# Kernel optimization log

Hardware: AMD Instinct MI355X
Metric: run time of the kernel (lower is better)

The kernel has to match this reference:

```python
import jax, jax.numpy as jnp
import numpy as np

N = 50000
E = 800000
F_IN = 1433
H = 256
C = 7


def setup_inputs() -> dict:
    key = jax.random.key(0)
    ks = jax.random.split(key, 8)
    x = jax.random.normal(ks[0], (N, F_IN), dtype=jnp.float32)
    edge_index = jax.random.randint(ks[1], (2, E), 0, N, dtype=jnp.int32)
    # glorot init for linear weights
    def glorot(k, fan_in, fan_out):
        s = jnp.sqrt(6.0 / (fan_in + fan_out)).astype(jnp.float32)
        return jax.random.uniform(k, (fan_in, fan_out), jnp.float32, -s, s)
    W1 = glorot(ks[2], F_IN, H)
    W2 = glorot(ks[3], H, H)
    W3 = glorot(ks[4], H, C)
    b1 = jnp.zeros((H,), jnp.float32)
    b2 = jnp.zeros((H,), jnp.float32)
    b3 = jnp.zeros((C,), jnp.float32)
    return {"x": x, "edge_index": edge_index, "W1": W1, "b1": b1,
            "W2": W2, "b2": b2, "W3": W3, "b3": b3}


def _gcn_norm(edge_index, num_nodes):
    # add self-loops, edge_weight = 1, symmetric normalization
    row = jnp.concatenate([edge_index[0], jnp.arange(num_nodes, dtype=edge_index.dtype)])
    col = jnp.concatenate([edge_index[1], jnp.arange(num_nodes, dtype=edge_index.dtype)])
    w = jnp.ones(row.shape[0], dtype=jnp.float32)
    deg = jax.ops.segment_sum(w, col, num_segments=num_nodes)  # degree on target (col)
    dinv = jnp.where(deg > 0, jax.lax.rsqrt(deg), 0.0)
    norm = dinv[row] * dinv[col]  # [E+N]
    return row, col, norm


def _gcn_layer(x, W, b, row, col, norm, num_nodes):
    h = x @ W                                   # [N, F_out]
    msg = h[row] * norm[:, None]                # gather + scale, [E+N, F_out]
    out = jax.ops.segment_sum(msg, col, num_segments=num_nodes)  # scatter-add
    return out + b


def reference(x, edge_index, W1, b1, W2, b2, W3, b3):
    row, col, norm = _gcn_norm(edge_index, N)
    h = jax.nn.relu(_gcn_layer(x, W1, b1, row, col, norm, N))
    h = jax.nn.relu(_gcn_layer(h, W2, b2, row, col, norm, N))
    h = _gcn_layer(h, W3, b3, row, col, norm, N)
    return jax.nn.log_softmax(h, axis=1)
```

## Files before the change

### kernel.cpp

```cpp
#include <hip/hip_runtime.h>
#include <math.h>

#define NNODES 50000
#define NEDGES 800000
#define FIN    1433
#define KP1    1472
#define HDIM   256
#define NCLS   7
#define MPAD   50048

typedef __attribute__((ext_vector_type(8))) short short8;
typedef __attribute__((ext_vector_type(4))) float f32x4;

__device__ __forceinline__ unsigned short f2bf(float f) {
    unsigned u = __builtin_bit_cast(unsigned, f);
    u += 0x7fffu + ((u >> 16) & 1u);
    return (unsigned short)(u >> 16);
}

__device__ __forceinline__ float bf2f(unsigned short u) {
    unsigned v = ((unsigned)u) << 16;
    return __builtin_bit_cast(float, v);
}

__device__ __forceinline__ void gl2lds16(const void* g, void* l) {
    __builtin_amdgcn_global_load_lds(
        (const __attribute__((address_space(1))) unsigned int*)g,
        (__attribute__((address_space(3))) unsigned int*)l, 16, 0, 0);
}


__global__ void count_kernel(const int* __restrict__ col, int* __restrict__ cnt, int E) {
    int e = blockIdx.x * blockDim.x + threadIdx.x;
    if (e < E) atomicAdd(&cnt[col[e]], 1);
}

__global__ __launch_bounds__(1024) void scan_kernel(const int* __restrict__ cnt,
                                                    int* __restrict__ rp,
                                                    float* __restrict__ dinv,
                                                    int n, int total) {
    __shared__ int sums[1024];
    int t = threadIdx.x;
    int chunk = (n + 1023) >> 10;
    int start = t * chunk;
    int end = start + chunk; if (end > n) end = n;
    int local = 0;
    for (int j = start; j < end; ++j) local += cnt[j];
    sums[t] = local;
    __syncthreads();
    for (int off = 1; off < 1024; off <<= 1) {
        int v = (t >= off) ? sums[t - off] : 0;
        __syncthreads();
        sums[t] += v;
        __syncthreads();
    }
    int run = (t == 0) ? 0 : sums[t - 1];
    for (int j = start; j < end; ++j) {
        int c = cnt[j];
        rp[j] = run; run += c;
        dinv[j] = rsqrtf((float)(c + 1));
    }
    if (t == 0) rp[n] = total;
}

__global__ void fill_kernel(const int* __restrict__ row, const int* __restrict__ col,
                            const int* __restrict__ rp, int* __restrict__ cur,
                            int* __restrict__ csr, float* __restrict__ wcsr,
                            const float* __restrict__ dinv, int E) {
    int e = blockIdx.x * blockDim.x + threadIdx.x;
    if (e < E) {
        int c = col[e], r = row[e];
        int pos = rp[c] + atomicAdd(&cur[c], 1);
        csr[pos] = r;
        wcsr[pos] = dinv[r] * dinv[c];
    }
}


__global__ void cast_wt_kernel(const float* __restrict__ W, unsigned short* __restrict__ Wt,
                               int Kin, int Kp, int Nn) {
    int idx = blockIdx.x * blockDim.x + threadIdx.x;
    if (idx >= Nn * Kp) return;
    int n = idx / Kp, k = idx % Kp;
    float f = (k < Kin) ? W[(size_t)k * Nn + n] : 0.f;
    Wt[idx] = f2bf(f);
}


__global__ __launch_bounds__(256) void gemm1_fused(const float* __restrict__ X,
                                                   const unsigned short* __restrict__ Bt,
                                                   unsigned short* __restrict__ C) {
    __shared__ __align__(16) unsigned short As[64 * 64];
    __shared__ __align__(16) unsigned short Bs[256 * 64];
    const int tid = threadIdx.x;
    const int wave = tid >> 6, lane = tid & 63;
    const int m0 = blockIdx.x * 64;
    const int wn = wave * 64;
    const int kq = lane >> 4, l16 = lane & 15, l8 = lane & 7, lh = lane >> 3;

    int rowbase[16];
    #pragma unroll
    for (int i = 0; i < 16; ++i) {
        int r = m0 + i * 4 + wave;
        if (r >= NNODES) r = NNODES - 1;
        rowbase[i] = r * FIN;
    }
    const int aw0 = wave * 64 + ((lh ^ wave) * 8) + l8;
    const int aw1 = wave * 64 + ((lh ^ (wave + 4)) * 8) + l8;

    int bo[8];
    #pragma unroll
    for (int i = 0; i < 8; ++i) {
        int c = i * 256 + tid;
        int n = c >> 3, ccg = (c & 7) ^ (n & 7);
        bo[i] = n * KP1 + ccg * 8;
    }

    int aoffb[2], boffb[2];
    #pragma unroll
    for (int ks = 0; ks < 2; ++ks) {
        int swz = ((ks * 4 + kq) ^ (l16 & 7)) * 8;
        aoffb[ks] = l16 * 64 + swz;
        boffb[ks] = (wn + l16) * 64 + swz;
    }

    f32x4 acc[4][4] = {};
    constexpr int NT = KP1 / 64;

    float fv[16];
    {
        #pragma unroll
        for (int i = 0; i < 16; ++i) fv[i] = X[rowbase[i] + lane];
    }

    for (int t = 0; t < NT; ++t) {
        const int k0 = t * 64;
        #pragma unroll
        for (int i = 0; i < 8; ++i)
            gl2lds16(Bt + bo[i] + k0, &Bs[(i * 256 + tid) * 8]);
        #pragma unroll
        for (int i = 0; i < 16; ++i)
            As[i * 256 + ((i & 1) ? aw1 : aw0)] = f2bf(fv[i]);
        __syncthreads();

        float nv[16];
        const bool more = (t + 1 < NT);
        if (more) {
            const int k = k0 + 64 + lane;
            const bool tail = (t + 2 == NT);
            #pragma unroll
            for (int i = 0; i < 16; ++i)
                nv[i] = (!tail || k < FIN) ? X[rowbase[i] + k] : 0.f;
        }

        #pragma unroll
        for (int ks = 0; ks < 2; ++ks) {
            short8 af[4], bg[4];
            #pragma unroll
            for (int i = 0; i < 4; ++i) af[i] = *(const short8*)&As[i * 1024 + aoffb[ks]];
            #pragma unroll
            for (int j = 0; j < 4; ++j) bg[j] = *(const short8*)&Bs[j * 1024 + boffb[ks]];
            #pragma unroll
            for (int i = 0; i < 4; ++i)
                #pragma unroll
                for (int j = 0; j < 4; ++j)
                    acc[i][j] = __builtin_amdgcn_mfma_f32_16x16x32_bf16(af[i], bg[j], acc[i][j], 0, 0, 0);
        }
        __syncthreads();
        if (more) {
            #pragma unroll
            for (int i = 0; i < 16; ++i) fv[i] = nv[i];
        }
    }

    #pragma unroll
    for (int i = 0; i < 4; ++i) {
        int gm_base = m0 + i * 16 + (lane >> 4) * 4;
        #pragma unroll
        for (int r = 0; r < 4; ++r) {
            int gm = gm_base + r;
            if (gm < NNODES) {
                #pragma unroll
                for (int j = 0; j < 4; ++j) {
                    int gn = wn + j * 16 + l16;
                    C[(size_t)gm * HDIM + gn] = f2bf(acc[i][j][r]);
                }
            }
        }
    }
}


__global__ __launch_bounds__(256) void gemm2_lds(const unsigned short* __restrict__ A,
                                                 const unsigned short* __restrict__ Bt,
                                                 unsigned short* __restrict__ C) {
    __shared__ __align__(16) unsigned short As[64 * 64];
    __shared__ __align__(16) unsigned short Bs[256 * 64];
    const int tid = threadIdx.x;
    const int wave = tid >> 6, lane = tid & 63;
    const int m0 = blockIdx.x * 64;
    const int wn = wave * 64;
    const int kq = lane >> 4, l16 = lane & 15;

    int ao[2];
    #pragma unroll
    for (int i = 0; i < 2; ++i) {
        int c = i * 256 + tid;
        int m = c >> 3, ccg = (c & 7) ^ (m & 7);
        ao[i] = (m0 + m) * HDIM + ccg * 8;
    }
    int bo[8];
    #pragma unroll
    for (int i = 0; i < 8; ++i) {
        int c = i * 256 + tid;
        int n = c >> 3, ccg = (c & 7) ^ (n & 7);
        bo[i] = n * HDIM + ccg * 8;
    }
    int aoffb[2], boffb[2];
    #pragma unroll
    for (int ks = 0; ks < 2; ++ks) {
        int swz = ((ks * 4 + kq) ^ (l16 & 7)) * 8;
        aoffb[ks] = l16 * 64 + swz;
        boffb[ks] = (wn + l16) * 64 + swz;
    }

    f32x4 acc[4][4] = {};
    #pragma unroll
    for (int k0 = 0; k0 < HDIM; k0 += 64) {
        #pragma unroll
        for (int i = 0; i < 2; ++i) gl2lds16(A + ao[i] + k0, &As[(i * 256 + tid) * 8]);
        #pragma unroll
        for (int i = 0; i < 8; ++i) gl2lds16(Bt + bo[i] + k0, &Bs[(i * 256 + tid) * 8]);
        __syncthreads();
        #pragma unroll
        for (int ks = 0; ks < 2; ++ks) {
            short8 af[4], bg[4];
            #pragma unroll
            for (int i = 0; i < 4; ++i) af[i] = *(const short8*)&As[i * 1024 + aoffb[ks]];
            #pragma unroll
            for (int j = 0; j < 4; ++j) bg[j] = *(const short8*)&Bs[j * 1024 + boffb[ks]];
            #pragma unroll
            for (int i = 0; i < 4; ++i)
                #pragma unroll
                for (int j = 0; j < 4; ++j)
                    acc[i][j] = __builtin_amdgcn_mfma_f32_16x16x32_bf16(af[i], bg[j], acc[i][j], 0, 0, 0);
        }
        __syncthreads();
    }

    #pragma unroll
    for (int i = 0; i < 4; ++i) {
        int gm_base = m0 + i * 16 + (lane >> 4) * 4;
        #pragma unroll
        for (int r = 0; r < 4; ++r) {
            int gm = gm_base + r;
            if (gm < NNODES) {
                #pragma unroll
                for (int j = 0; j < 4; ++j) {
                    int gn = wn + j * 16 + l16;
                    C[(size_t)gm * HDIM + gn] = f2bf(acc[i][j][r]);
                }
            }
        }
    }
}


__device__ __forceinline__ void aggregate_row(const ushort4* __restrict__ h, int lane,
                                              int p, int p1,
                                              const int* __restrict__ csr,
                                              const float* __restrict__ wcsr,
                                              float& ax, float& ay, float& az, float& aw) {
    for (; p + 8 <= p1; p += 8) {
        int s[8]; float wv[8];
        #pragma unroll
        for (int j = 0; j < 8; ++j) { s[j] = csr[p + j]; wv[j] = wcsr[p + j]; }
        ushort4 t[8];
        #pragma unroll
        for (int j = 0; j < 8; ++j) t[j] = h[s[j] * 64 + lane];
        #pragma unroll
        for (int j = 0; j < 8; ++j) {
            ax += wv[j] * bf2f(t[j].x); ay += wv[j] * bf2f(t[j].y);
            az += wv[j] * bf2f(t[j].z); aw += wv[j] * bf2f(t[j].w);
        }
    }
    if (p + 4 <= p1) {
        int s[4]; float wv[4];
        #pragma unroll
        for (int j = 0; j < 4; ++j) { s[j] = csr[p + j]; wv[j] = wcsr[p + j]; }
        ushort4 t[4];
        #pragma unroll
        for (int j = 0; j < 4; ++j) t[j] = h[s[j] * 64 + lane];
        #pragma unroll
        for (int j = 0; j < 4; ++j) {
            ax += wv[j] * bf2f(t[j].x); ay += wv[j] * bf2f(t[j].y);
            az += wv[j] * bf2f(t[j].z); aw += wv[j] * bf2f(t[j].w);
        }
        p += 4;
    }
    for (; p < p1; ++p) {
        int s = csr[p];
        float wg = wcsr[p];
        ushort4 t = h[s * 64 + lane];
        ax += wg * bf2f(t.x); ay += wg * bf2f(t.y); az += wg * bf2f(t.z); aw += wg * bf2f(t.w);
    }
}


__global__ __launch_bounds__(256) void agg_kernel(const ushort4* __restrict__ h,
                                                  ushort4* __restrict__ out,
                                                  const float* __restrict__ dinv,
                                                  const int* __restrict__ rp,
                                                  const int* __restrict__ csr,
                                                  const float* __restrict__ wcsr,
                                                  const float* __restrict__ bias,
                                                  int n) {
    int node = blockIdx.x * 4 + (threadIdx.x >> 6);
    int lane = threadIdx.x & 63;
    if (node >= n) return;
    float di = dinv[node];
    float sw = di * di;
    ushort4 hv = h[node * 64 + lane];
    float ax = sw * bf2f(hv.x), ay = sw * bf2f(hv.y);
    float az = sw * bf2f(hv.z), aw = sw * bf2f(hv.w);
    aggregate_row(h, lane, rp[node], rp[node + 1], csr, wcsr, ax, ay, az, aw);
    float4 b = ((const float4*)bias)[lane];
    ax = fmaxf(ax + b.x, 0.f); ay = fmaxf(ay + b.y, 0.f);
    az = fmaxf(az + b.z, 0.f); aw = fmaxf(aw + b.w, 0.f);
    out[node * 64 + lane] = make_ushort4(f2bf(ax), f2bf(ay), f2bf(az), f2bf(aw));
}


__global__ __launch_bounds__(256) void agg2_mm3_kernel(const ushort4* __restrict__ h,
                                                       float* __restrict__ h3,
                                                       const float* __restrict__ dinv,
                                                       const int* __restrict__ rp,
                                                       const int* __restrict__ csr,
                                                       const float* __restrict__ wcsr,
                                                       const float* __restrict__ bias,
                                                       const float* __restrict__ W3,
                                                       int n) {
    __shared__ __align__(16) float Ws[NCLS * HDIM];
    int tid = threadIdx.x;
    for (int i = tid; i < NCLS * HDIM; i += 256)
        Ws[i] = W3[(i & 255) * NCLS + (i >> 8)];
    __syncthreads();

    int node = blockIdx.x * 4 + (tid >> 6);
    int lane = tid & 63;
    if (node >= n) return;
    float di = dinv[node];
    float sw = di * di;
    ushort4 hv = h[node * 64 + lane];
    float ax = sw * bf2f(hv.x), ay = sw * bf2f(hv.y);
    float az = sw * bf2f(hv.z), aw = sw * bf2f(hv.w);
    aggregate_row(h, lane, rp[node], rp[node + 1], csr, wcsr, ax, ay, az, aw);
    float4 b = ((const float4*)bias)[lane];
    ax = fmaxf(ax + b.x, 0.f); ay = fmaxf(ay + b.y, 0.f);
    az = fmaxf(az + b.z, 0.f); aw = fmaxf(aw + b.w, 0.f);

    float p7[NCLS];
    #pragma unroll
    for (int c = 0; c < NCLS; ++c) {
        float4 w4 = *(const float4*)&Ws[c * HDIM + 4 * lane];
        p7[c] = ax * w4.x + ay * w4.y + az * w4.z + aw * w4.w;
    }
    #pragma unroll
    for (int c = 0; c < NCLS; ++c)
        for (int off = 32; off > 0; off >>= 1) p7[c] += __shfl_down(p7[c], off);
    if (lane == 0) {
        #pragma unroll
        for (int c = 0; c < NCLS; ++c) h3[node * NCLS + c] = p7[c];
    }
}


__global__ void final_kernel(const float* __restrict__ h3, const float* __restrict__ dinv,
                             const int* __restrict__ rp, const int* __restrict__ csr,
                             const float* __restrict__ wcsr,
                             const float* __restrict__ b3, float* __restrict__ out, int n) {
    int i = blockIdx.x * blockDim.x + threadIdx.x;
    if (i >= n) return;
    float di = dinv[i];
    float sw = di * di;
    float acc[NCLS];
    #pragma unroll
    for (int c = 0; c < NCLS; ++c) acc[c] = sw * h3[i * NCLS + c];
    int p = rp[i], p1 = rp[i + 1];
    for (; p + 4 <= p1; p += 4) {
        int s0 = csr[p], s1 = csr[p + 1], s2 = csr[p + 2], s3 = csr[p + 3];
        float w0 = wcsr[p], w1 = wcsr[p + 1], w2 = wcsr[p + 2], w3 = wcsr[p + 3];
        #pragma unroll
        for (int c = 0; c < NCLS; ++c)
            acc[c] += w0 * h3[s0 * NCLS + c] + w1 * h3[s1 * NCLS + c]
                    + w2 * h3[s2 * NCLS + c] + w3 * h3[s3 * NCLS + c];
    }
    for (; p < p1; ++p) {
        int s = csr[p];
        float wg = wcsr[p];
        #pragma unroll
        for (int c = 0; c < NCLS; ++c) acc[c] += wg * h3[s * NCLS + c];
    }
    float mx = -1e30f;
    #pragma unroll
    for (int c = 0; c < NCLS; ++c) { acc[c] += b3[c]; mx = fmaxf(mx, acc[c]); }
    float sum = 0.f;
    #pragma unroll
    for (int c = 0; c < NCLS; ++c) sum += expf(acc[c] - mx);
    float lse = mx + logf(sum);
    #pragma unroll
    for (int c = 0; c < NCLS; ++c) out[i * NCLS + c] = acc[c] - lse;
}


extern "C" void kernel_launch(void* const* d_in, const int* in_sizes, int n_in,
                              void* d_out, int out_size, void* d_ws, size_t ws_size,
                              hipStream_t stream) {
    const float* x  = (const float*)d_in[0];
    const int*   ei = (const int*)d_in[1];
    const float* W1 = (const float*)d_in[2];
    const float* b1 = (const float*)d_in[3];
    const float* W2 = (const float*)d_in[4];
    const float* b2 = (const float*)d_in[5];
    const float* W3 = (const float*)d_in[6];
    const float* b3 = (const float*)d_in[7];
    float* out = (float*)d_out;
    const int* row = ei;
    const int* col = ei + NEDGES;

    char* w = (char*)d_ws;
    auto alloc = [&](size_t b) { void* p = (void*)w; w += (b + 255) & ~(size_t)255; return p; };
    int*   cnt  = (int*)alloc(NNODES * 4);
    int*   cur  = (int*)alloc(NNODES * 4);
    int*   rp   = (int*)alloc((NNODES + 1) * 4);
    float* dinv = (float*)alloc(NNODES * 4);
    int*   csr  = (int*)alloc((size_t)NEDGES * 4);
    float* wcsr = (float*)alloc((size_t)NEDGES * 4);
    unsigned short* w1t  = (unsigned short*)alloc((size_t)HDIM * KP1 * 2);
    unsigned short* w2t  = (unsigned short*)alloc((size_t)HDIM * HDIM * 2);
    unsigned short* h_bf = (unsigned short*)alloc((size_t)MPAD * HDIM * 2);
    unsigned short* a_bf = (unsigned short*)alloc((size_t)MPAD * HDIM * 2);
    float* h3 = (float*)alloc((size_t)NNODES * NCLS * 4);

    hipMemsetAsync(cnt, 0, NNODES * 4, stream);
    hipMemsetAsync(cur, 0, NNODES * 4, stream);
    count_kernel<<<(NEDGES + 255) / 256, 256, 0, stream>>>(col, cnt, NEDGES);
    scan_kernel<<<1, 1024, 0, stream>>>(cnt, rp, dinv, NNODES, NEDGES);
    fill_kernel<<<(NEDGES + 255) / 256, 256, 0, stream>>>(row, col, rp, cur, csr, wcsr, dinv, NEDGES);

    cast_wt_kernel<<<(HDIM * KP1 + 255) / 256, 256, 0, stream>>>(W1, w1t, FIN, KP1, HDIM);
    cast_wt_kernel<<<(HDIM * HDIM + 255) / 256, 256, 0, stream>>>(W2, w2t, HDIM, HDIM, HDIM);

    gemm1_fused<<<MPAD / 64, 256, 0, stream>>>(x, w1t, h_bf);
    agg_kernel<<<(NNODES + 3) / 4, 256, 0, stream>>>((const ushort4*)h_bf, (ushort4*)a_bf,
                                                     dinv, rp, csr, wcsr, b1, NNODES);
    gemm2_lds<<<MPAD / 64, 256, 0, stream>>>(a_bf, w2t, h_bf);
    agg2_mm3_kernel<<<(NNODES + 3) / 4, 256, 0, stream>>>((const ushort4*)h_bf, h3,
                                                          dinv, rp, csr, wcsr, b2, W3, NNODES);
    final_kernel<<<(NNODES + 255) / 256, 256, 0, stream>>>(h3, dinv, rp, csr, wcsr, b3, out, NNODES);
}
```

Measured before the change: 783.3 us.

## Parallelize CSR scan, interleave edge index/weight, vectorize X loads in GEMM1

Replaces the single-block serial scan with a three-kernel multi-block scan (partial sums, top scan, apply). Packs CSR source index and edge weight into one int2 array so each edge is fetched with a single 8-byte load in all aggregation kernels. GEMM1 now loads X with 16-byte float4 reads, each lane covering 4 consecutive columns, and writes packed ushort4 bf16 into the LDS A tile using a new swizzle. It also merges the two weight-cast launches and the two memsets into one each, adding some launch and code complexity in exchange.

```diff
diff --git a/kernel.cpp b/kernel.cpp
--- a/kernel.cpp
+++ b/kernel.cpp
@@ -29,61 +29,97 @@
         (__attribute__((address_space(3))) unsigned int*)l, 16, 0, 0);
 }
 
+__device__ __forceinline__ f32x4 ld4u(const float* p) {
+    f32x4 v; __builtin_memcpy(&v, p, 16); return v;
+}
+
 
 __global__ void count_kernel(const int* __restrict__ col, int* __restrict__ cnt, int E) {
     int e = blockIdx.x * blockDim.x + threadIdx.x;
     if (e < E) atomicAdd(&cnt[col[e]], 1);
 }
 
-__global__ __launch_bounds__(1024) void scan_kernel(const int* __restrict__ cnt,
-                                                    int* __restrict__ rp,
-                                                    float* __restrict__ dinv,
-                                                    int n, int total) {
-    __shared__ int sums[1024];
+#define SCAN_BS 512
+
+__global__ __launch_bounds__(SCAN_BS) void scan_part(const int* __restrict__ cnt,
+                                                     int* __restrict__ bsum, int n) {
+    __shared__ int red[SCAN_BS];
     int t = threadIdx.x;
-    int chunk = (n + 1023) >> 10;
-    int start = t * chunk;
-    int end = start + chunk; if (end > n) end = n;
-    int local = 0;
-    for (int j = start; j < end; ++j) local += cnt[j];
-    sums[t] = local;
+    int i = blockIdx.x * SCAN_BS + t;
+    red[t] = (i < n) ? cnt[i] : 0;
     __syncthreads();
-    for (int off = 1; off < 1024; off <<= 1) {
-        int v = (t >= off) ? sums[t - off] : 0;
-        __syncthreads();
-        sums[t] += v;
-        __syncthreads();
-    }
-    int run = (t == 0) ? 0 : sums[t - 1];
-    for (int j = start; j < end; ++j) {
-        int c = cnt[j];
-        rp[j] = run; run += c;
-        dinv[j] = rsqrtf((float)(c + 1));
-    }
-    if (t == 0) rp[n] = total;
+    for (int off = SCAN_BS / 2; off > 0; off >>= 1) {
+        if (t < off) red[t] += red[t + off];
+        __syncthreads();
+    }
+    if (t == 0) bsum[blockIdx.x] = red[0];
+}
+
+__global__ __launch_bounds__(128) void scan_top(int* __restrict__ bsum, int nb) {
+    __shared__ int s[128];
+    int t = threadIdx.x;
+    int v = (t < nb) ? bsum[t] : 0;
+    s[t] = v;
+    __syncthreads();
+    for (int off = 1; off < 128; off <<= 1) {
+        int u = (t >= off) ? s[t - off] : 0;
+        __syncthreads();
+        s[t] += u;
+        __syncthreads();
+    }
+    if (t < nb) bsum[t] = s[t] - v;
+}
+
+__global__ __launch_bounds__(SCAN_BS) void scan_apply(const int* __restrict__ cnt,
+                                                      const int* __restrict__ bsum,
+                                                      int* __restrict__ rp,
+                                                      float* __restrict__ dinv,
+                                                      int n, int total) {
+    __shared__ int s[SCAN_BS];
+    int t = threadIdx.x;
+    int i = blockIdx.x * SCAN_BS + t;
+    int v = (i < n) ? cnt[i] : 0;
+    s[t] = v;
+    __syncthreads();
+    for (int off = 1; off < SCAN_BS; off <<= 1) {
+        int u = (t >= off) ? s[t - off] : 0;
+        __syncthreads();
+        s[t] += u;
+        __syncthreads();
+    }
+    if (i < n) {
+        rp[i] = bsum[blockIdx.x] + s[t] - v;
+        dinv[i] = rsqrtf((float)(v + 1));
+    }
+    if (i == n) rp[n] = total;
 }
 
 __global__ void fill_kernel(const int* __restrict__ row, const int* __restrict__ col,
                             const int* __restrict__ rp, int* __restrict__ cur,
-                            int* __restrict__ csr, float* __restrict__ wcsr,
+                            int2* __restrict__ csrw,
                             const float* __restrict__ dinv, int E) {
     int e = blockIdx.x * blockDim.x + threadIdx.x;
     if (e < E) {
         int c = col[e], r = row[e];
         int pos = rp[c] + atomicAdd(&cur[c], 1);
-        csr[pos] = r;
-        wcsr[pos] = dinv[r] * dinv[c];
-    }
-}
-
-
-__global__ void cast_wt_kernel(const float* __restrict__ W, unsigned short* __restrict__ Wt,
-                               int Kin, int Kp, int Nn) {
+        csrw[pos] = make_int2(r, __float_as_int(dinv[r] * dinv[c]));
+    }
+}
+
+
+__global__ void cast_wt2(const float* __restrict__ W1, const float* __restrict__ W2,
+                         unsigned short* __restrict__ w1t, unsigned short* __restrict__ w2t) {
     int idx = blockIdx.x * blockDim.x + threadIdx.x;
-    if (idx >= Nn * Kp) return;
-    int n = idx / Kp, k = idx % Kp;
-    float f = (k < Kin) ? W[(size_t)k * Nn + n] : 0.f;
-    Wt[idx] = f2bf(f);
+    if (idx < HDIM * KP1) {
+        int n = idx / KP1, k = idx % KP1;
+        w1t[idx] = f2bf((k < FIN) ? W1[(size_t)k * HDIM + n] : 0.f);
+    } else {
+        int j = idx - HDIM * KP1;
+        if (j < HDIM * HDIM) {
+            int n = j / HDIM, k = j % HDIM;
+            w2t[j] = f2bf(W2[(size_t)k * HDIM + n]);
+        }
+    }
 }
 
 
@@ -96,17 +132,23 @@
     const int wave = tid >> 6, lane = tid & 63;
     const int m0 = blockIdx.x * 64;
     const int wn = wave * 64;
-    const int kq = lane >> 4, l16 = lane & 15, l8 = lane & 7, lh = lane >> 3;
-
-    int rowbase[16];
-    #pragma unroll
-    for (int i = 0; i < 16; ++i) {
-        int r = m0 + i * 4 + wave;
+    const int kq = lane >> 4, l16 = lane & 15;
+    const int lq = lane >> 4;
+    const int h  = lane & 15;
+
+    int rowbase[4];
+    #pragma unroll
+    for (int i = 0; i < 4; ++i) {
+        int r = m0 + wave * 16 + i * 4 + lq;
         if (r >= NNODES) r = NNODES - 1;
         rowbase[i] = r * FIN;
     }
-    const int aw0 = wave * 64 + ((lh ^ wave) * 8) + l8;
-    const int aw1 = wave * 64 + ((lh ^ (wave + 4)) * 8) + l8;
+    int aw[4];
+    #pragma unroll
+    for (int i = 0; i < 4; ++i) {
+        int r7 = lq + 4 * (i & 1);
+        aw[i] = (wave * 16 + i * 4 + lq) * 64 + (((h >> 1) ^ r7) * 8) + (h & 1) * 4;
+    }
 
     int bo[8];
     #pragma unroll
@@ -127,11 +169,9 @@
     f32x4 acc[4][4] = {};
     constexpr int NT = KP1 / 64;
 
-    float fv[16];
-    {
-        #pragma unroll
-        for (int i = 0; i < 16; ++i) fv[i] = X[rowbase[i] + lane];
-    }
+    f32x4 fv[4];
+    #pragma unroll
+    for (int i = 0; i < 4; ++i) fv[i] = ld4u(&X[rowbase[i] + h * 4]);
 
     for (int t = 0; t < NT; ++t) {
         const int k0 = t * 64;
@@ -139,18 +179,30 @@
         for (int i = 0; i < 8; ++i)
             gl2lds16(Bt + bo[i] + k0, &Bs[(i * 256 + tid) * 8]);
         #pragma unroll
-        for (int i = 0; i < 16; ++i)
-            As[i * 256 + ((i & 1) ? aw1 : aw0)] = f2bf(fv[i]);
-        __syncthreads();
-
-        float nv[16];
+        for (int i = 0; i < 4; ++i) {
+            ushort4 pk = make_ushort4(f2bf(fv[i].x), f2bf(fv[i].y),
+                                      f2bf(fv[i].z), f2bf(fv[i].w));
+            *(ushort4*)&As[aw[i]] = pk;
+        }
+        __syncthreads();
+
+        f32x4 nv[4];
         const bool more = (t + 1 < NT);
         if (more) {
-            const int k = k0 + 64 + lane;
-            const bool tail = (t + 2 == NT);
-            #pragma unroll
-            for (int i = 0; i < 16; ++i)
-                nv[i] = (!tail || k < FIN) ? X[rowbase[i] + k] : 0.f;
+            const int kb = k0 + 64 + h * 4;
+            if (t + 2 == NT) {
+                #pragma unroll
+                for (int i = 0; i < 4; ++i) {
+                    float a = (kb + 0 < FIN) ? X[rowbase[i] + kb + 0] : 0.f;
+                    float b = (kb + 1 < FIN) ? X[rowbase[i] + kb + 1] : 0.f;
+                    float c = (kb + 2 < FIN) ? X[rowbase[i] + kb + 2] : 0.f;
+                    float d = (kb + 3 < FIN) ? X[rowbase[i] + kb + 3] : 0.f;
+                    nv[i] = (f32x4){a, b, c, d};
+                }
+            } else {
+                #pragma unroll
+                for (int i = 0; i < 4; ++i) nv[i] = ld4u(&X[rowbase[i] + kb]);
+            }
         }
 
         #pragma unroll
@@ -169,7 +221,7 @@
         __syncthreads();
         if (more) {
             #pragma unroll
-            for (int i = 0; i < 16; ++i) fv[i] = nv[i];
+            for (int i = 0; i < 4; ++i) fv[i] = nv[i];
         }
     }
 
@@ -268,41 +320,42 @@
 
 __device__ __forceinline__ void aggregate_row(const ushort4* __restrict__ h, int lane,
                                               int p, int p1,
-                                              const int* __restrict__ csr,
-                                              const float* __restrict__ wcsr,
+                                              const int2* __restrict__ csrw,
                                               float& ax, float& ay, float& az, float& aw) {
     for (; p + 8 <= p1; p += 8) {
-        int s[8]; float wv[8];
-        #pragma unroll
-        for (int j = 0; j < 8; ++j) { s[j] = csr[p + j]; wv[j] = wcsr[p + j]; }
+        int2 e[8];
+        #pragma unroll
+        for (int j = 0; j < 8; ++j) e[j] = csrw[p + j];
         ushort4 t[8];
         #pragma unroll
-        for (int j = 0; j < 8; ++j) t[j] = h[s[j] * 64 + lane];
+        for (int j = 0; j < 8; ++j) t[j] = h[e[j].x * 64 + lane];
         #pragma unroll
         for (int j = 0; j < 8; ++j) {
-            ax += wv[j] * bf2f(t[j].x); ay += wv[j] * bf2f(t[j].y);
-            az += wv[j] * bf2f(t[j].z); aw += wv[j] * bf2f(t[j].w);
+            float w = __int_as_float(e[j].y);
+            ax += w * bf2f(t[j].x); ay += w * bf2f(t[j].y);
+            az += w * bf2f(t[j].z); aw += w * bf2f(t[j].w);
         }
     }
     if (p + 4 <= p1) {
-        int s[4]; float wv[4];
-        #pragma unroll
-        for (int j = 0; j < 4; ++j) { s[j] = csr[p + j]; wv[j] = wcsr[p + j]; }
+        int2 e[4];
+        #pragma unroll
+        for (int j = 0; j < 4; ++j) e[j] = csrw[p + j];
         ushort4 t[4];
         #pragma unroll
-        for (int j = 0; j < 4; ++j) t[j] = h[s[j] * 64 + lane];
+        for (int j = 0; j < 4; ++j) t[j] = h[e[j].x * 64 + lane];
         #pragma unroll
         for (int j = 0; j < 4; ++j) {
-            ax += wv[j] * bf2f(t[j].x); ay += wv[j] * bf2f(t[j].y);
-            az += wv[j] * bf2f(t[j].z); aw += wv[j] * bf2f(t[j].w);
+            float w = __int_as_float(e[j].y);
+            ax += w * bf2f(t[j].x); ay += w * bf2f(t[j].y);
+            az += w * bf2f(t[j].z); aw += w * bf2f(t[j].w);
         }
         p += 4;
     }
     for (; p < p1; ++p) {
-        int s = csr[p];
-        float wg = wcsr[p];
-        ushort4 t = h[s * 64 + lane];
-        ax += wg * bf2f(t.x); ay += wg * bf2f(t.y); az += wg * bf2f(t.z); aw += wg * bf2f(t.w);
+        int2 e = csrw[p];
+        float w = __int_as_float(e.y);
+        ushort4 t = h[e.x * 64 + lane];
+        ax += w * bf2f(t.x); ay += w * bf2f(t.y); az += w * bf2f(t.z); aw += w * bf2f(t.w);
     }
 }
 
@@ -311,8 +364,7 @@
                                                   ushort4* __restrict__ out,
                                                   const float* __restrict__ dinv,
                                                   const int* __restrict__ rp,
-                                                  const int* __restrict__ csr,
-                                                  const float* __restrict__ wcsr,
+                                                  const int2* __restrict__ csrw,
                                                   const float* __restrict__ bias,
                                                   int n) {
     int node = blockIdx.x * 4 + (threadIdx.x >> 6);
@@ -323,7 +375,7 @@
     ushort4 hv = h[node * 64 + lane];
     float ax = sw * bf2f(hv.x), ay = sw * bf2f(hv.y);
     float az = sw * bf2f(hv.z), aw = sw * bf2f(hv.w);
-    aggregate_row(h, lane, rp[node], rp[node + 1], csr, wcsr, ax, ay, az, aw);
+    aggregate_row(h, lane, rp[node], rp[node + 1], csrw, ax, ay, az, aw);
     float4 b = ((const float4*)bias)[lane];
     ax = fmaxf(ax + b.x, 0.f); ay = fmaxf(ay + b.y, 0.f);
     az = fmaxf(az + b.z, 0.f); aw = fmaxf(aw + b.w, 0.f);
@@ -335,8 +387,7 @@
                                                        float* __restrict__ h3,
                                                        const float* __restrict__ dinv,
                                                        const int* __restrict__ rp,
-                                                       const int* __restrict__ csr,
-                                                       const float* __restrict__ wcsr,
+                                                       const int2* __restrict__ csrw,
                                                        const float* __restrict__ bias,
                                                        const float* __restrict__ W3,
                                                        int n) {
@@ -354,7 +405,7 @@
     ushort4 hv = h[node * 64 + lane];
     float ax = sw * bf2f(hv.x), ay = sw * bf2f(hv.y);
     float az = sw * bf2f(hv.z), aw = sw * bf2f(hv.w);
-    aggregate_row(h, lane, rp[node], rp[node + 1], csr, wcsr, ax, ay, az, aw);
+    aggregate_row(h, lane, rp[node], rp[node + 1], csrw, ax, ay, az, aw);
     float4 b = ((const float4*)bias)[lane];
     ax = fmaxf(ax + b.x, 0.f); ay = fmaxf(ay + b.y, 0.f);
     az = fmaxf(az + b.z, 0.f); aw = fmaxf(aw + b.w, 0.f);
@@ -376,8 +427,7 @@
 
 
 __global__ void final_kernel(const float* __restrict__ h3, const float* __restrict__ dinv,
-                             const int* __restrict__ rp, const int* __restrict__ csr,
-                             const float* __restrict__ wcsr,
+                             const int* __restrict__ rp, const int2* __restrict__ csrw,
                              const float* __restrict__ b3, float* __restrict__ out, int n) {
     int i = blockIdx.x * blockDim.x + threadIdx.x;
     if (i >= n) return;
@@ -388,18 +438,19 @@
     for (int c = 0; c < NCLS; ++c) acc[c] = sw * h3[i * NCLS + c];
     int p = rp[i], p1 = rp[i + 1];
     for (; p + 4 <= p1; p += 4) {
-        int s0 = csr[p], s1 = csr[p + 1], s2 = csr[p + 2], s3 = csr[p + 3];
-        float w0 = wcsr[p], w1 = wcsr[p + 1], w2 = wcsr[p + 2], w3 = wcsr[p + 3];
+        int2 e0 = csrw[p], e1 = csrw[p + 1], e2 = csrw[p + 2], e3 = csrw[p + 3];
+        float w0 = __int_as_float(e0.y), w1 = __int_as_float(e1.y);
+        float w2 = __int_as_float(e2.y), w3 = __int_as_float(e3.y);
         #pragma unroll
         for (int c = 0; c < NCLS; ++c)
-            acc[c] += w0 * h3[s0 * NCLS + c] + w1 * h3[s1 * NCLS + c]
-                    + w2 * h3[s2 * NCLS + c] + w3 * h3[s3 * NCLS + c];
+            acc[c] += w0 * h3[e0.x * NCLS + c] + w1 * h3[e1.x * NCLS + c]
+                    + w2 * h3[e2.x * NCLS + c] + w3 * h3[e3.x * NCLS + c];
     }
     for (; p < p1; ++p) {
-        int s = csr[p];
-        float wg = wcsr[p];
-        #pragma unroll
-        for (int c = 0; c < NCLS; ++c) acc[c] += wg * h3[s * NCLS + c];
+        int2 e = csrw[p];
+        float wg = __int_as_float(e.y);
+        #pragma unroll
+        for (int c = 0; c < NCLS; ++c) acc[c] += wg * h3[e.x * NCLS + c];
     }
     float mx = -1e30f;
     #pragma unroll
@@ -434,28 +485,31 @@
     int*   cur  = (int*)alloc(NNODES * 4);
     int*   rp   = (int*)alloc((NNODES + 1) * 4);
     float* dinv = (float*)alloc(NNODES * 4);
-    int*   csr  = (int*)alloc((size_t)NEDGES * 4);
-    float* wcsr = (float*)alloc((size_t)NEDGES * 4);
+    int*   bsum = (int*)alloc(128 * 4);
+    int2*  csrw = (int2*)alloc((size_t)NEDGES * 8);
     unsigned short* w1t  = (unsigned short*)alloc((size_t)HDIM * KP1 * 2);
     unsigned short* w2t  = (unsigned short*)alloc((size_t)HDIM * HDIM * 2);
     unsigned short* h_bf = (unsigned short*)alloc((size_t)MPAD * HDIM * 2);
     unsigned short* a_bf = (unsigned short*)alloc((size_t)MPAD * HDIM * 2);
     float* h3 = (float*)alloc((size_t)NNODES * NCLS * 4);
 
-    hipMemsetAsync(cnt, 0, NNODES * 4, stream);
-    hipMemsetAsync(cur, 0, NNODES * 4, stream);
+    const size_t cpad = ((size_t)NNODES * 4 + 255) & ~(size_t)255;
+    hipMemsetAsync(cnt, 0, cpad + (size_t)NNODES * 4, stream);
+
     count_kernel<<<(NEDGES + 255) / 256, 256, 0, stream>>>(col, cnt, NEDGES);
-    scan_kernel<<<1, 1024, 0, stream>>>(cnt, rp, dinv, NNODES, NEDGES);
-    fill_kernel<<<(NEDGES + 255) / 256, 256, 0, stream>>>(row, col, rp, cur, csr, wcsr, dinv, NEDGES);
-
-    cast_wt_kernel<<<(HDIM * KP1 + 255) / 256, 256, 0, stream>>>(W1, w1t, FIN, KP1, HDIM);
-    cast_wt_kernel<<<(HDIM * HDIM + 255) / 256, 256, 0, stream>>>(W2, w2t, HDIM, HDIM, HDIM);
+    const int nsb = (NNODES + SCAN_BS - 1) / SCAN_BS;
+    scan_part <<<nsb, SCAN_BS, 0, stream>>>(cnt, bsum, NNODES);
+    scan_top  <<<1, 128, 0, stream>>>(bsum, nsb);
+    scan_apply<<<nsb, SCAN_BS, 0, stream>>>(cnt, bsum, rp, dinv, NNODES, NEDGES);
+    fill_kernel<<<(NEDGES + 255) / 256, 256, 0, stream>>>(row, col, rp, cur, csrw, dinv, NEDGES);
+
+    cast_wt2<<<(HDIM * KP1 + HDIM * HDIM + 255) / 256, 256, 0, stream>>>(W1, W2, w1t, w2t);
 
     gemm1_fused<<<MPAD / 64, 256, 0, stream>>>(x, w1t, h_bf);
     agg_kernel<<<(NNODES + 3) / 4, 256, 0, stream>>>((const ushort4*)h_bf, (ushort4*)a_bf,
-                                                     dinv, rp, csr, wcsr, b1, NNODES);
+                                                     dinv, rp, csrw, b1, NNODES);
     gemm2_lds<<<MPAD / 64, 256, 0, stream>>>(a_bf, w2t, h_bf);
     agg2_mm3_kernel<<<(NNODES + 3) / 4, 256, 0, stream>>>((const ushort4*)h_bf, h3,
-                                                          dinv, rp, csr, wcsr, b2, W3, NNODES);
-    final_kernel<<<(NNODES + 255) / 256, 256, 0, stream>>>(h3, dinv, rp, csr, wcsr, b3, out, NNODES);
-}
+                                                          dinv, rp, csrw, b2, W3, NNODES);
+    final_kernel<<<(NNODES + 255) / 256, 256, 0, stream>>>(h3, dinv, rp, csrw, b3, out, NNODES);
+}
```

Result: faster. 676.8 us (-13.6%).
